# Performance work log

Measured on AMD Instinct MI355X. Metric: run time of the kernel, lower is better.

The kernel has to match this reference:

```python
import jax, jax.numpy as jnp
import numpy as np

N = 50000
E = 600000
OB_DIM = 128
H = 128
P_OUT = 8


def _glorot(key, fan_in, fan_out):
    lim = float(np.sqrt(6.0 / (fan_in + fan_out)))
    return jax.random.uniform(key, (fan_in, fan_out), jnp.float32, -lim, lim)


def setup_inputs() -> dict:
    key = jax.random.key(0)
    ks = jax.random.split(key, 16)
    x = jax.random.normal(ks[0], (N, OB_DIM), jnp.float32)
    edge_index = jax.random.randint(ks[1], (2, E), 0, N, jnp.int64)
    dims = [(OB_DIM, H), (H, H), (H, P_OUT), (OB_DIM, H), (H, H), (H, 1)]
    names = ["p1", "p2", "p3", "v1", "v2", "v3"]
    inp = {"x": x, "edge_index": edge_index}
    for i, (nm, (fi, fo)) in enumerate(zip(names, dims)):
        inp["W" + nm] = _glorot(ks[2 + i], fi, fo)
        inp["b" + nm] = jnp.zeros((fo,), jnp.float32)
    return inp


def _gcn_norm(edge_index, n):
    # add self-loops, symmetric normalization deg^{-1/2} A_hat deg^{-1/2}
    loops = jnp.arange(n, dtype=edge_index.dtype)
    src = jnp.concatenate([edge_index[0], loops])
    dst = jnp.concatenate([edge_index[1], loops])
    deg = jax.ops.segment_sum(jnp.ones_like(dst, jnp.float32), dst, num_segments=n)
    dinv = jax.lax.rsqrt(jnp.maximum(deg, 1.0))
    norm = dinv[src] * dinv[dst]  # [E+N]
    return src, dst, norm


def _gcn_conv(x, W, b, src, dst, norm, n):
    h = x @ W                      # [N, out]
    msg = h[src] * norm[:, None]   # gather + scale, [E+N, out]
    out = jax.ops.segment_sum(msg, dst, num_segments=n)
    return out + b


def reference(x, edge_index, Wp1, bp1, Wp2, bp2, Wp3, bp3, Wv1, bv1, Wv2, bv2, Wv3, bv3):
    n = x.shape[0]
    src, dst, norm = _gcn_norm(edge_index, n)
    # policy branch
    a = jax.nn.relu(_gcn_conv(x, Wp1, bp1, src, dst, norm, n))
    a = jax.nn.relu(_gcn_conv(a, Wp2, bp2, src, dst, norm, n))
    action_logits = _gcn_conv(a, Wp3, bp3, src, dst, norm, n)  # Categorical logits
    # value branch
    v = jax.nn.relu(_gcn_conv(x, Wv1, bv1, src, dst, norm, n))
    v = jax.nn.relu(_gcn_conv(v, Wv2, bv2, src, dst, norm, n))
    v = _gcn_conv(v, Wv3, bv3, src, dst, norm, n)
    return action_logits, v
```

## Files before the change

kernel.cpp:

```cpp
#include <hip/hip_runtime.h>

#define NN 50000
#define NE 600000

typedef unsigned short ushort_t;
typedef ushort_t ushortx8 __attribute__((ext_vector_type(8)));
typedef ushort_t ushortx4 __attribute__((ext_vector_type(4)));
typedef short bf16x8 __attribute__((ext_vector_type(8)));
typedef float f32x4 __attribute__((ext_vector_type(4)));
typedef int intx2 __attribute__((ext_vector_type(2)));
typedef float fltx4 __attribute__((ext_vector_type(4)));

__device__ __forceinline__ float bf2f(ushort_t u) {
    union { unsigned int i; float f; } c;
    c.i = ((unsigned int)u) << 16;
    return c.f;
}
__device__ __forceinline__ ushort_t f2bf(float f) {
    union { float f; unsigned int i; } c;
    c.f = f;
    unsigned int u = c.i;
    unsigned int r = u + 0x7FFFu + ((u >> 16) & 1u);
    return (ushort_t)(r >> 16);
}
__device__ __forceinline__ unsigned cvtpk(float lo, float hi) {
    unsigned r;
    asm("v_cvt_pk_bf16_f32 %0, %1, %2" : "=v"(r) : "v"(lo), "v"(hi));
    return r;
}

__global__ void k_pre(const float* __restrict__ X, ushort_t* __restrict__ XB,
                      const int* __restrict__ ei, int* __restrict__ cnt) {
    int b = blockIdx.x;
    if (b < 3125) {
        size_t i = (size_t)b * 256 + threadIdx.x;
        const float4* X4 = (const float4*)X;
        float4 a = X4[i * 2], c4 = X4[i * 2 + 1];
        union { unsigned u[4]; ushortx8 v; } cv;
        cv.u[0] = cvtpk(a.x, a.y);
        cv.u[1] = cvtpk(a.z, a.w);
        cv.u[2] = cvtpk(c4.x, c4.y);
        cv.u[3] = cvtpk(c4.z, c4.w);
        __builtin_nontemporal_store(cv.v, (ushortx8*)XB + i);
    } else {
        int e = (b - 3125) * 256 + threadIdx.x;
        if (e < NE) {
            int d = __builtin_nontemporal_load(ei + NE + e);
            atomicAdd(&cnt[d], 1);
        }
    }
}

__global__ void k_scan1(const int* __restrict__ cnt, int* __restrict__ rowptr,
                        int* __restrict__ bsum, float* __restrict__ dinv) {
    __shared__ int s[256];
    int t = threadIdx.x;
    int i = blockIdx.x * 256 + t;
    int v = (i < NN) ? cnt[i] : 0;
    if (i < NN) dinv[i] = rsqrtf(1.0f + (float)v);
    s[t] = v;
    __syncthreads();
    for (int d = 1; d < 256; d <<= 1) {
        int tmp = (t >= d) ? s[t - d] : 0;
        __syncthreads();
        s[t] += tmp;
        __syncthreads();
    }
    if (i < NN) rowptr[i] = s[t] - v;
    if (t == 255) bsum[blockIdx.x] = s[255];
}

__global__ void k_scan2_prep(int* __restrict__ bsum, int* __restrict__ boff, int nb,
                             const float* __restrict__ Wp1, const float* __restrict__ Wv1,
                             const float* __restrict__ Wp2, const float* __restrict__ Wv2,
                             ushort_t* __restrict__ Wt1, ushort_t* __restrict__ Wt2p,
                             ushort_t* __restrict__ Wt2v) {
    int b = blockIdx.x, t = threadIdx.x;
    if (b < 128) {
        int idx = b * 256 + t;
        int n = idx >> 7, k = idx & 127;
        float v = (n < 128) ? Wp1[k * 128 + n] : Wv1[k * 128 + (n - 128)];
        Wt1[n * 128 + k] = f2bf(v);
    } else if (b < 192) {
        int idx = (b - 128) * 256 + t;
        int n = idx >> 7, k = idx & 127;
        Wt2p[n * 128 + k] = f2bf(Wp2[k * 128 + n]);
    } else if (b < 256) {
        int idx = (b - 192) * 256 + t;
        int n = idx >> 7, k = idx & 127;
        Wt2v[n * 128 + k] = f2bf(Wv2[k * 128 + n]);
    } else {
        __shared__ int s[256];
        int v = (t < nb) ? bsum[t] : 0;
        s[t] = v;
        __syncthreads();
        for (int d = 1; d < 256; d <<= 1) {
            int tmp = (t >= d) ? s[t - d] : 0;
            __syncthreads();
            s[t] += tmp;
            __syncthreads();
        }
        boff[t] = s[t] - v;
    }
}

__global__ void k_scan3rc(const int* __restrict__ rowptr, const int* __restrict__ cnt,
                          const int* __restrict__ boff, int2* __restrict__ rc) {
    int i = blockIdx.x * 256 + threadIdx.x;
    if (i < NN) {
        int2 v;
        v.x = rowptr[i] + boff[blockIdx.x];
        v.y = cnt[i];
        rc[i] = v;
    }
}

__global__ void k_fill(const int* __restrict__ ei, const int2* __restrict__ rc,
                       int* __restrict__ fill, const float* __restrict__ dinv,
                       int2* __restrict__ edges) {
    int e = blockIdx.x * 256 + threadIdx.x;
    if (e < NE) {
        int s = __builtin_nontemporal_load(ei + e);
        int d = __builtin_nontemporal_load(ei + NE + e);
        int pos = rc[d].x + atomicAdd(&fill[d], 1);
        int2 pr;
        pr.x = s;
        pr.y = __float_as_int(dinv[s] * dinv[d]);
        edges[pos] = pr;
    }
}

__global__ __launch_bounds__(256) void k_agg128(const ushort_t* __restrict__ H,
                                                ushort_t* __restrict__ OUT,
                                                const float* __restrict__ dinv,
                                                const int2* __restrict__ rc,
                                                const int2* __restrict__ edges) {
    int wv = threadIdx.x >> 6;
    int l = threadIdx.x & 63;
    int i = blockIdx.x * 4 + wv;
    if (i >= NN) return;
    int t2 = l >> 4, q = l & 15;
    const ushortx8* H8 = (const ushortx8*)H;

    float a0[8] = {}, a1[8] = {};
    float di = dinv[i];
    float ws = (t2 == 0) ? di * di : 0.f;
    ushortx8 hv = H8[(size_t)i * 16 + q];
#pragma unroll
    for (int k = 0; k < 8; ++k) a0[k] = ws * bf2f(hv[k]);

    int2 rcv = rc[i];
    int st = rcv.x, n = rcv.y;

    for (int j = t2; j < n; j += 16) {
        int idx[4];
        float w[4];
#pragma unroll
        for (int s = 0; s < 4; ++s) {
            int jj = j + 4 * s;
            bool valid = jj < n;
            intx2 em = __builtin_nontemporal_load(
                (const intx2*)edges + (valid ? st + jj : st));
            idx[s] = valid ? em.x : i;
            w[s] = valid ? __int_as_float(em.y) : 0.f;
        }
        ushortx8 hh[4];
#pragma unroll
        for (int s = 0; s < 4; ++s) hh[s] = H8[(size_t)idx[s] * 16 + q];
#pragma unroll
        for (int k = 0; k < 8; ++k) a0[k] += w[0] * bf2f(hh[0][k]);
#pragma unroll
        for (int k = 0; k < 8; ++k) a1[k] += w[1] * bf2f(hh[1][k]);
#pragma unroll
        for (int k = 0; k < 8; ++k) a0[k] += w[2] * bf2f(hh[2][k]);
#pragma unroll
        for (int k = 0; k < 8; ++k) a1[k] += w[3] * bf2f(hh[3][k]);
    }
#pragma unroll
    for (int k = 0; k < 8; ++k) a0[k] += a1[k];
#pragma unroll
    for (int k = 0; k < 8; ++k) {
        a0[k] += __shfl_xor(a0[k], 16, 64);
        a0[k] += __shfl_xor(a0[k], 32, 64);
    }
    if (l < 16) {
        ushortx8 o = {f2bf(a0[0]), f2bf(a0[1]), f2bf(a0[2]), f2bf(a0[3]),
                      f2bf(a0[4]), f2bf(a0[5]), f2bf(a0[6]), f2bf(a0[7])};
        __builtin_nontemporal_store(o, (ushortx8*)OUT + (size_t)i * 16 + q);
    }
}

__global__ __launch_bounds__(256) void k_agg256(const ushort_t* __restrict__ H,
                                                ushort_t* __restrict__ OUT,
                                                const float* __restrict__ dinv,
                                                const int2* __restrict__ rc,
                                                const int2* __restrict__ edges) {
    int wv = threadIdx.x >> 6;
    int l = threadIdx.x & 63;
    int i = blockIdx.x * 4 + wv;
    if (i >= NN) return;
    int h = l >> 5, q = l & 31;
    const ushortx8* H8 = (const ushortx8*)H;

    float a0[8] = {}, a1[8] = {};
    float di = dinv[i];
    float ws = (h == 0) ? di * di : 0.f;
    ushortx8 hv = H8[(size_t)i * 32 + q];
#pragma unroll
    for (int k = 0; k < 8; ++k) a0[k] = ws * bf2f(hv[k]);

    int2 rcv = rc[i];
    int st = rcv.x, n = rcv.y;

    for (int j = h; j < n; j += 8) {
        int idx[4];
        float w[4];
#pragma unroll
        for (int s = 0; s < 4; ++s) {
            int jj = j + 2 * s;
            bool valid = jj < n;
            intx2 em = __builtin_nontemporal_load(
                (const intx2*)edges + (valid ? st + jj : st));
            idx[s] = valid ? em.x : i;
            w[s] = valid ? __int_as_float(em.y) : 0.f;
        }
        ushortx8 hh[4];
#pragma unroll
        for (int s = 0; s < 4; ++s) hh[s] = H8[(size_t)idx[s] * 32 + q];
#pragma unroll
        for (int k = 0; k < 8; ++k) a0[k] += w[0] * bf2f(hh[0][k]);
#pragma unroll
        for (int k = 0; k < 8; ++k) a1[k] += w[1] * bf2f(hh[1][k]);
#pragma unroll
        for (int k = 0; k < 8; ++k) a0[k] += w[2] * bf2f(hh[2][k]);
#pragma unroll
        for (int k = 0; k < 8; ++k) a1[k] += w[3] * bf2f(hh[3][k]);
    }
#pragma unroll
    for (int k = 0; k < 8; ++k) a0[k] += a1[k];
#pragma unroll
    for (int k = 0; k < 8; ++k) a0[k] += __shfl_xor(a0[k], 32, 64);

    if (h == 0) {
        ushortx8 o = {f2bf(a0[0]), f2bf(a0[1]), f2bf(a0[2]), f2bf(a0[3]),
                      f2bf(a0[4]), f2bf(a0[5]), f2bf(a0[6]), f2bf(a0[7])};
        __builtin_nontemporal_store(o, (ushortx8*)OUT + (size_t)i * 32 + q);
    }
}

__global__ __launch_bounds__(256) void k_gemm1(const ushort_t* __restrict__ A,
                                               const ushort_t* __restrict__ Wt1,
                                               const float* __restrict__ bL,
                                               const float* __restrict__ bH,
                                               ushort_t* __restrict__ C, int nrows) {
    __shared__ ushort_t Wl[256 * 128];
    int t = threadIdx.x;
    const ushortx8* Wg = (const ushortx8*)Wt1;
#pragma unroll
    for (int i = 0; i < 16; ++i) {
        int c = i * 256 + t;
        int row = c >> 4, slot = c & 15;
        int db = row * 256 + ((slot * 16) ^ ((row & 7) << 4));
        *(ushortx8*)((char*)Wl + db) = Wg[c];
    }
    __syncthreads();

    int w = t >> 6, l = t & 63, m = l & 15, g = l >> 4;
    int r0 = blockIdx.x * 64 + w * 16;
    if (r0 >= nrows) return;

    const ushort_t* Arow = A + (size_t)(r0 + m) * 128;
    bf16x8 af[4];
#pragma unroll
    for (int kk = 0; kk < 4; ++kk) af[kk] = *(const bf16x8*)(Arow + kk * 32 + g * 8);

    f32x4 acc[16];
#pragma unroll
    for (int nt = 0; nt < 16; ++nt) acc[nt] = (f32x4){0.f, 0.f, 0.f, 0.f};
    int sw = (m & 7) << 4;
#pragma unroll
    for (int nt = 0; nt < 16; ++nt) {
        const char* Wb = (const char*)Wl + (nt * 16 + m) * 256;
#pragma unroll
        for (int kk = 0; kk < 4; ++kk) {
            bf16x8 wf = *(const bf16x8*)(Wb + ((kk * 64 + g * 16) ^ sw));
            acc[nt] = __builtin_amdgcn_mfma_f32_16x16x32_bf16(wf, af[kk], acc[nt], 0, 0, 0);
        }
    }
#pragma unroll
    for (int nt = 0; nt < 16; ++nt) {
        const float* bb = (nt < 8) ? (bL + nt * 16 + g * 4) : (bH + (nt - 8) * 16 + g * 4);
        float4 bv = *(const float4*)bb;
        ushortx4 o = {f2bf(fmaxf(acc[nt][0] + bv.x, 0.f)),
                      f2bf(fmaxf(acc[nt][1] + bv.y, 0.f)),
                      f2bf(fmaxf(acc[nt][2] + bv.z, 0.f)),
                      f2bf(fmaxf(acc[nt][3] + bv.w, 0.f))};
        *(ushortx4*)(C + (size_t)(r0 + m) * 256 + nt * 16 + g * 4) = o;
    }
}

__global__ __launch_bounds__(256) void k_gemm2s(const ushort_t* __restrict__ A,
                                                const ushort_t* __restrict__ Wp,
                                                const ushort_t* __restrict__ Wv,
                                                const float* __restrict__ bL,
                                                const float* __restrict__ bH,
                                                const float* __restrict__ Wp3,
                                                const float* __restrict__ Wv3,
                                                float* __restrict__ FS, int nrows) {
    __shared__ ushort_t Wl[2 * 128 * 128];
    __shared__ float W3c[9][128];
    int t = threadIdx.x;
    const ushortx8* Wgp = (const ushortx8*)Wp;
    const ushortx8* Wgv = (const ushortx8*)Wv;
#pragma unroll
    for (int i = 0; i < 8; ++i) {
        int c = i * 256 + t;
        int row = c >> 4, slot = c & 15;
        int db = row * 256 + ((slot * 16) ^ ((row & 7) << 4));
        *(ushortx8*)((char*)Wl + db) = Wgp[c];
        *(ushortx8*)((char*)Wl + 32768 + db) = Wgv[c];
    }
    for (int jj = t; jj < 1152; jj += 256) {
        int c = jj >> 7, k = jj & 127;
        W3c[c][k] = (c < 8) ? Wp3[k * 8 + c] : Wv3[k];
    }
    __syncthreads();

    int w = t >> 6, l = t & 63, m = l & 15, g = l >> 4;
    int r0 = blockIdx.x * 64 + w * 16;
    if (r0 >= nrows) return;

    const ushort_t* Arow = A + (size_t)(r0 + m) * 256;
    bf16x8 alo[4], ahi[4];
#pragma unroll
    for (int kk = 0; kk < 4; ++kk) {
        alo[kk] = *(const bf16x8*)(Arow + kk * 32 + g * 8);
        ahi[kk] = *(const bf16x8*)(Arow + 128 + kk * 32 + g * 8);
    }

    f32x4 accp[8], accv[8];
#pragma unroll
    for (int nt = 0; nt < 8; ++nt) {
        accp[nt] = (f32x4){0.f, 0.f, 0.f, 0.f};
        accv[nt] = (f32x4){0.f, 0.f, 0.f, 0.f};
    }
    int sw = (m & 7) << 4;
#pragma unroll
    for (int nt = 0; nt < 8; ++nt) {
        const char* Wbp = (const char*)Wl + (nt * 16 + m) * 256;
        const char* Wbv = Wbp + 32768;
#pragma unroll
        for (int kk = 0; kk < 4; ++kk) {
            int off = (kk * 64 + g * 16) ^ sw;
            bf16x8 wfp = *(const bf16x8*)(Wbp + off);
            accp[nt] = __builtin_amdgcn_mfma_f32_16x16x32_bf16(wfp, alo[kk], accp[nt], 0, 0, 0);
            bf16x8 wfv = *(const bf16x8*)(Wbv + off);
            accv[nt] = __builtin_amdgcn_mfma_f32_16x16x32_bf16(wfv, ahi[kk], accv[nt], 0, 0, 0);
        }
    }

    float rp[8][4], rv[8][4];
#pragma unroll
    for (int nt = 0; nt < 8; ++nt) {
        float4 bp = *(const float4*)(bL + nt * 16 + g * 4);
        float4 bv = *(const float4*)(bH + nt * 16 + g * 4);
        rp[nt][0] = fmaxf(accp[nt][0] + bp.x, 0.f);
        rp[nt][1] = fmaxf(accp[nt][1] + bp.y, 0.f);
        rp[nt][2] = fmaxf(accp[nt][2] + bp.z, 0.f);
        rp[nt][3] = fmaxf(accp[nt][3] + bp.w, 0.f);
        rv[nt][0] = fmaxf(accv[nt][0] + bv.x, 0.f);
        rv[nt][1] = fmaxf(accv[nt][1] + bv.y, 0.f);
        rv[nt][2] = fmaxf(accv[nt][2] + bv.z, 0.f);
        rv[nt][3] = fmaxf(accv[nt][3] + bv.w, 0.f);
    }

    float ps[9] = {};
#pragma unroll
    for (int c = 0; c < 8; ++c) {
#pragma unroll
        for (int nt = 0; nt < 8; ++nt) {
            float4 w4 = *(const float4*)&W3c[c][nt * 16 + g * 4];
            ps[c] += rp[nt][0] * w4.x + rp[nt][1] * w4.y + rp[nt][2] * w4.z + rp[nt][3] * w4.w;
        }
    }
#pragma unroll
    for (int nt = 0; nt < 8; ++nt) {
        float4 w4 = *(const float4*)&W3c[8][nt * 16 + g * 4];
        ps[8] += rv[nt][0] * w4.x + rv[nt][1] * w4.y + rv[nt][2] * w4.z + rv[nt][3] * w4.w;
    }
#pragma unroll
    for (int c = 0; c < 9; ++c) {
        ps[c] += __shfl_xor(ps[c], 16, 64);
        ps[c] += __shfl_xor(ps[c], 32, 64);
    }
    if (g == 0) {
        float* o = FS + (size_t)(r0 + m) * 12;
        fltx4 o0 = {ps[0], ps[1], ps[2], ps[3]};
        fltx4 o1 = {ps[4], ps[5], ps[6], ps[7]};
        __builtin_nontemporal_store(o0, (fltx4*)o);
        __builtin_nontemporal_store(o1, (fltx4*)o + 1);
        __builtin_nontemporal_store(ps[8], o + 8);
    }
}

__global__ void k_agg9(const float* __restrict__ FS, float* __restrict__ out_logits,
                       float* __restrict__ out_v, const float* __restrict__ bp3,
                       const float* __restrict__ bv3, const float* __restrict__ dinv,
                       const int2* __restrict__ rc, const int2* __restrict__ edges) {
    int i = blockIdx.x * 256 + threadIdx.x;
    if (i >= NN) return;
    float di = dinv[i];
    float w0 = di * di;
    const float4* F = (const float4*)FS;
    size_t b0 = (size_t)i * 3;
    float4 x0 = F[b0], x1 = F[b0 + 1], x2 = F[b0 + 2];
    float a[9];
    a[0] = w0 * x0.x; a[1] = w0 * x0.y; a[2] = w0 * x0.z; a[3] = w0 * x0.w;
    a[4] = w0 * x1.x; a[5] = w0 * x1.y; a[6] = w0 * x1.z; a[7] = w0 * x1.w;
    a[8] = w0 * x2.x;
    int2 rcv = rc[i];
    int st = rcv.x, n = rcv.y;
    for (int j = 0; j < n; ++j) {
        int2 e = edges[st + j];
        float w = __int_as_float(e.y);
        size_t sb = (size_t)e.x * 3;
        float4 y0 = F[sb], y1 = F[sb + 1], y2 = F[sb + 2];
        a[0] += w * y0.x; a[1] += w * y0.y; a[2] += w * y0.z; a[3] += w * y0.w;
        a[4] += w * y1.x; a[5] += w * y1.y; a[6] += w * y1.z; a[7] += w * y1.w;
        a[8] += w * y2.x;
    }
    float4 bpa = *(const float4*)bp3;
    float4 bpb = *(const float4*)(bp3 + 4);
    fltx4 o0 = {a[0] + bpa.x, a[1] + bpa.y, a[2] + bpa.z, a[3] + bpa.w};
    fltx4 o1 = {a[4] + bpb.x, a[5] + bpb.y, a[6] + bpb.z, a[7] + bpb.w};
    __builtin_nontemporal_store(o0, (fltx4*)out_logits + (size_t)i * 2);
    __builtin_nontemporal_store(o1, (fltx4*)out_logits + (size_t)i * 2 + 1);
    __builtin_nontemporal_store(a[8] + bv3[0], out_v + i);
}

extern "C" void kernel_launch(void* const* d_in, const int* in_sizes, int n_in,
                              void* d_out, int out_size, void* d_ws, size_t ws_size,
                              hipStream_t stream) {
    const float* x   = (const float*)d_in[0];
    const int*   ei  = (const int*)d_in[1];
    const float* Wp1 = (const float*)d_in[2],  *bp1 = (const float*)d_in[3];
    const float* Wp2 = (const float*)d_in[4],  *bp2 = (const float*)d_in[5];
    const float* Wp3 = (const float*)d_in[6],  *bp3 = (const float*)d_in[7];
    const float* Wv1 = (const float*)d_in[8],  *bv1 = (const float*)d_in[9];
    const float* Wv2 = (const float*)d_in[10], *bv2 = (const float*)d_in[11];
    const float* Wv3 = (const float*)d_in[12], *bv3 = (const float*)d_in[13];
    float* out_logits = (float*)d_out;
    float* out_v = (float*)d_out + (size_t)NN * 8;

    char* w = (char*)d_ws;
    auto alloc = [&](size_t bytes) {
        char* p = w;
        w += (bytes + 255) & ~(size_t)255;
        return p;
    };
    int*      cntfill = (int*)alloc((size_t)2 * NN * 4);
    int*      cnt    = cntfill;
    int*      fill   = cntfill + NN;
    int*      rowptr = (int*)alloc(NN * 4);
    int*      bsum   = (int*)alloc(256 * 4);
    int*      boff   = (int*)alloc(256 * 4);
    float*    dinv   = (float*)alloc(NN * 4);
    int2*     rc     = (int2*)alloc((size_t)NN * 8);
    int2*     edges  = (int2*)alloc((size_t)NE * 8);
    ushort_t* Wt1    = (ushort_t*)alloc(256 * 128 * 2);
    ushort_t* Wt2p   = (ushort_t*)alloc(128 * 128 * 2);
    ushort_t* Wt2v   = (ushort_t*)alloc(128 * 128 * 2);
    ushort_t* xb     = (ushort_t*)alloc((size_t)NN * 128 * 2);
    ushort_t* ag0    = (ushort_t*)alloc((size_t)NN * 128 * 2);
    ushort_t* f1b    = (ushort_t*)alloc((size_t)NN * 256 * 2);
    ushort_t* ag1    = (ushort_t*)alloc((size_t)NN * 256 * 2);
    float*    fs     = (float*)alloc((size_t)NN * 12 * 4);

    const int NB = (NN + 255) / 256;
    const int EB = (NE + 255) / 256;
    const int GB = (NN + 63) / 64;
    const int AB = NN / 4;

    (void)hipMemsetAsync(cntfill, 0, (size_t)2 * NN * 4, stream);
    k_pre<<<3125 + EB, 256, 0, stream>>>(x, xb, ei, cnt);
    k_scan1<<<NB, 256, 0, stream>>>(cnt, rowptr, bsum, dinv);
    k_scan2_prep<<<257, 256, 0, stream>>>(bsum, boff, NB, Wp1, Wv1, Wp2, Wv2,
                                          Wt1, Wt2p, Wt2v);
    k_scan3rc<<<NB, 256, 0, stream>>>(rowptr, cnt, boff, rc);
    k_fill<<<EB, 256, 0, stream>>>(ei, rc, fill, dinv, edges);

    k_agg128<<<AB, 256, 0, stream>>>(xb, ag0, dinv, rc, edges);
    k_gemm1<<<GB, 256, 0, stream>>>(ag0, Wt1, bp1, bv1, f1b, NN);
    k_agg256<<<AB, 256, 0, stream>>>(f1b, ag1, dinv, rc, edges);
    k_gemm2s<<<GB, 256, 0, stream>>>(ag1, Wt2p, Wt2v, bp2, bv2, Wp3, Wv3, fs, NN);
    k_agg9<<<NB, 256, 0, stream>>>(fs, out_logits, out_v, bp3, bv3, dinv, rc, edges);
}
```

Before: 207.0 us.

## Merge CSR scan kernels with atomic block offsets and fold weight prep into preprocess

The three-kernel prefix scan becomes a single kernel. Each block takes its global row offset from an atomic counter, which leaves CSR segments out of node order but still valid. The weight transpose and bf16 conversion move into the preprocessing kernel, cutting two launches and their serialization. Nontemporal stores on intermediates become regular stores so later kernels can hit them in cache, and the final feature buffer is padded from 12 to 16 floats per row for aligned gathers. The costs are non-deterministic edge ordering across nodes and extra memory for the padded buffer.

```diff
diff --git a/kernel.cpp b/kernel.cpp
--- a/kernel.cpp
+++ b/kernel.cpp
@@ -2,6 +2,7 @@
 
 #define NN 50000
 #define NE 600000
+#define EBLK 2344
 
 typedef unsigned short ushort_t;
 typedef ushort_t ushortx8 __attribute__((ext_vector_type(8)));
@@ -30,10 +31,14 @@
 }
 
 __global__ void k_pre(const float* __restrict__ X, ushort_t* __restrict__ XB,
-                      const int* __restrict__ ei, int* __restrict__ cnt) {
-    int b = blockIdx.x;
+                      const int* __restrict__ ei, int* __restrict__ cnt,
+                      const float* __restrict__ Wp1, const float* __restrict__ Wv1,
+                      const float* __restrict__ Wp2, const float* __restrict__ Wv2,
+                      ushort_t* __restrict__ Wt1, ushort_t* __restrict__ Wt2p,
+                      ushort_t* __restrict__ Wt2v) {
+    int b = blockIdx.x, t = threadIdx.x;
     if (b < 3125) {
-        size_t i = (size_t)b * 256 + threadIdx.x;
+        size_t i = (size_t)b * 256 + t;
         const float4* X4 = (const float4*)X;
         float4 a = X4[i * 2], c4 = X4[i * 2 + 1];
         union { unsigned u[4]; ushortx8 v; } cv;
@@ -41,19 +46,36 @@
         cv.u[1] = cvtpk(a.z, a.w);
         cv.u[2] = cvtpk(c4.x, c4.y);
         cv.u[3] = cvtpk(c4.z, c4.w);
-        __builtin_nontemporal_store(cv.v, (ushortx8*)XB + i);
-    } else {
-        int e = (b - 3125) * 256 + threadIdx.x;
+        ((ushortx8*)XB)[i] = cv.v;
+    } else if (b < 3125 + EBLK) {
+        int e = (b - 3125) * 256 + t;
         if (e < NE) {
             int d = __builtin_nontemporal_load(ei + NE + e);
             atomicAdd(&cnt[d], 1);
         }
-    }
-}
-
-__global__ void k_scan1(const int* __restrict__ cnt, int* __restrict__ rowptr,
-                        int* __restrict__ bsum, float* __restrict__ dinv) {
+    } else {
+        int wb = b - 3125 - EBLK;
+        if (wb < 128) {
+            int idx = wb * 256 + t;
+            int n = idx >> 7, k = idx & 127;
+            float v = (n < 128) ? Wp1[k * 128 + n] : Wv1[k * 128 + (n - 128)];
+            Wt1[n * 128 + k] = f2bf(v);
+        } else if (wb < 192) {
+            int idx = (wb - 128) * 256 + t;
+            int n = idx >> 7, k = idx & 127;
+            Wt2p[n * 128 + k] = f2bf(Wp2[k * 128 + n]);
+        } else {
+            int idx = (wb - 192) * 256 + t;
+            int n = idx >> 7, k = idx & 127;
+            Wt2v[n * 128 + k] = f2bf(Wv2[k * 128 + n]);
+        }
+    }
+}
+
+__global__ void k_scanrc(const int* __restrict__ cnt, float* __restrict__ dinv,
+                         int2* __restrict__ rc, int* __restrict__ gofs) {
     __shared__ int s[256];
+    __shared__ int base;
     int t = threadIdx.x;
     int i = blockIdx.x * 256 + t;
     int v = (i < NN) ? cnt[i] : 0;
@@ -66,52 +88,13 @@
         s[t] += tmp;
         __syncthreads();
     }
-    if (i < NN) rowptr[i] = s[t] - v;
-    if (t == 255) bsum[blockIdx.x] = s[255];
-}
-
-__global__ void k_scan2_prep(int* __restrict__ bsum, int* __restrict__ boff, int nb,
-                             const float* __restrict__ Wp1, const float* __restrict__ Wv1,
-                             const float* __restrict__ Wp2, const float* __restrict__ Wv2,
-                             ushort_t* __restrict__ Wt1, ushort_t* __restrict__ Wt2p,
-                             ushort_t* __restrict__ Wt2v) {
-    int b = blockIdx.x, t = threadIdx.x;
-    if (b < 128) {
-        int idx = b * 256 + t;
-        int n = idx >> 7, k = idx & 127;
-        float v = (n < 128) ? Wp1[k * 128 + n] : Wv1[k * 128 + (n - 128)];
-        Wt1[n * 128 + k] = f2bf(v);
-    } else if (b < 192) {
-        int idx = (b - 128) * 256 + t;
-        int n = idx >> 7, k = idx & 127;
-        Wt2p[n * 128 + k] = f2bf(Wp2[k * 128 + n]);
-    } else if (b < 256) {
-        int idx = (b - 192) * 256 + t;
-        int n = idx >> 7, k = idx & 127;
-        Wt2v[n * 128 + k] = f2bf(Wv2[k * 128 + n]);
-    } else {
-        __shared__ int s[256];
-        int v = (t < nb) ? bsum[t] : 0;
-        s[t] = v;
-        __syncthreads();
-        for (int d = 1; d < 256; d <<= 1) {
-            int tmp = (t >= d) ? s[t - d] : 0;
-            __syncthreads();
-            s[t] += tmp;
-            __syncthreads();
-        }
-        boff[t] = s[t] - v;
-    }
-}
-
-__global__ void k_scan3rc(const int* __restrict__ rowptr, const int* __restrict__ cnt,
-                          const int* __restrict__ boff, int2* __restrict__ rc) {
-    int i = blockIdx.x * 256 + threadIdx.x;
+    if (t == 255) base = atomicAdd(gofs, s[255]);
+    __syncthreads();
     if (i < NN) {
-        int2 v;
-        v.x = rowptr[i] + boff[blockIdx.x];
-        v.y = cnt[i];
-        rc[i] = v;
+        int2 o;
+        o.x = base + s[t] - v;
+        o.y = v;
+        rc[i] = o;
     }
 }
 
@@ -186,7 +169,7 @@
     if (l < 16) {
         ushortx8 o = {f2bf(a0[0]), f2bf(a0[1]), f2bf(a0[2]), f2bf(a0[3]),
                       f2bf(a0[4]), f2bf(a0[5]), f2bf(a0[6]), f2bf(a0[7])};
-        __builtin_nontemporal_store(o, (ushortx8*)OUT + (size_t)i * 16 + q);
+        ((ushortx8*)OUT)[(size_t)i * 16 + q] = o;
     }
 }
 
@@ -244,7 +227,7 @@
     if (h == 0) {
         ushortx8 o = {f2bf(a0[0]), f2bf(a0[1]), f2bf(a0[2]), f2bf(a0[3]),
                       f2bf(a0[4]), f2bf(a0[5]), f2bf(a0[6]), f2bf(a0[7])};
-        __builtin_nontemporal_store(o, (ushortx8*)OUT + (size_t)i * 32 + q);
+        ((ushortx8*)OUT)[(size_t)i * 32 + q] = o;
     }
 }
 
@@ -394,12 +377,10 @@
         ps[c] += __shfl_xor(ps[c], 32, 64);
     }
     if (g == 0) {
-        float* o = FS + (size_t)(r0 + m) * 12;
-        fltx4 o0 = {ps[0], ps[1], ps[2], ps[3]};
-        fltx4 o1 = {ps[4], ps[5], ps[6], ps[7]};
-        __builtin_nontemporal_store(o0, (fltx4*)o);
-        __builtin_nontemporal_store(o1, (fltx4*)o + 1);
-        __builtin_nontemporal_store(ps[8], o + 8);
+        float* o = FS + (size_t)(r0 + m) * 16;
+        *(fltx4*)o = (fltx4){ps[0], ps[1], ps[2], ps[3]};
+        *(fltx4*)(o + 4) = (fltx4){ps[4], ps[5], ps[6], ps[7]};
+        o[8] = ps[8];
     }
 }
 
@@ -412,22 +393,24 @@
     float di = dinv[i];
     float w0 = di * di;
     const float4* F = (const float4*)FS;
-    size_t b0 = (size_t)i * 3;
-    float4 x0 = F[b0], x1 = F[b0 + 1], x2 = F[b0 + 2];
+    size_t b0 = (size_t)i * 4;
+    float4 x0 = F[b0], x1 = F[b0 + 1];
+    float x2 = FS[(size_t)i * 16 + 8];
     float a[9];
     a[0] = w0 * x0.x; a[1] = w0 * x0.y; a[2] = w0 * x0.z; a[3] = w0 * x0.w;
     a[4] = w0 * x1.x; a[5] = w0 * x1.y; a[6] = w0 * x1.z; a[7] = w0 * x1.w;
-    a[8] = w0 * x2.x;
+    a[8] = w0 * x2;
     int2 rcv = rc[i];
     int st = rcv.x, n = rcv.y;
     for (int j = 0; j < n; ++j) {
         int2 e = edges[st + j];
         float w = __int_as_float(e.y);
-        size_t sb = (size_t)e.x * 3;
-        float4 y0 = F[sb], y1 = F[sb + 1], y2 = F[sb + 2];
+        size_t sb = (size_t)e.x * 4;
+        float4 y0 = F[sb], y1 = F[sb + 1];
+        float y2 = FS[(size_t)e.x * 16 + 8];
         a[0] += w * y0.x; a[1] += w * y0.y; a[2] += w * y0.z; a[3] += w * y0.w;
         a[4] += w * y1.x; a[5] += w * y1.y; a[6] += w * y1.z; a[7] += w * y1.w;
-        a[8] += w * y2.x;
+        a[8] += w * y2;
     }
     float4 bpa = *(const float4*)bp3;
     float4 bpb = *(const float4*)(bp3 + 4);
@@ -458,12 +441,10 @@
         w += (bytes + 255) & ~(size_t)255;
         return p;
     };
-    int*      cntfill = (int*)alloc((size_t)2 * NN * 4);
-    int*      cnt    = cntfill;
-    int*      fill   = cntfill + NN;
-    int*      rowptr = (int*)alloc(NN * 4);
-    int*      bsum   = (int*)alloc(256 * 4);
-    int*      boff   = (int*)alloc(256 * 4);
+    int*      zeroed = (int*)alloc(((size_t)2 * NN + 256) * 4);
+    int*      cnt    = zeroed;
+    int*      fill   = zeroed + NN;
+    int*      gofs   = zeroed + 2 * NN;
     float*    dinv   = (float*)alloc(NN * 4);
     int2*     rc     = (int2*)alloc((size_t)NN * 8);
     int2*     edges  = (int2*)alloc((size_t)NE * 8);
@@ -474,20 +455,17 @@
     ushort_t* ag0    = (ushort_t*)alloc((size_t)NN * 128 * 2);
     ushort_t* f1b    = (ushort_t*)alloc((size_t)NN * 256 * 2);
     ushort_t* ag1    = (ushort_t*)alloc((size_t)NN * 256 * 2);
-    float*    fs     = (float*)alloc((size_t)NN * 12 * 4);
+    float*    fs     = (float*)alloc((size_t)NN * 16 * 4);
 
     const int NB = (NN + 255) / 256;
-    const int EB = (NE + 255) / 256;
     const int GB = (NN + 63) / 64;
     const int AB = NN / 4;
 
-    (void)hipMemsetAsync(cntfill, 0, (size_t)2 * NN * 4, stream);
-    k_pre<<<3125 + EB, 256, 0, stream>>>(x, xb, ei, cnt);
-    k_scan1<<<NB, 256, 0, stream>>>(cnt, rowptr, bsum, dinv);
-    k_scan2_prep<<<257, 256, 0, stream>>>(bsum, boff, NB, Wp1, Wv1, Wp2, Wv2,
-                                          Wt1, Wt2p, Wt2v);
-    k_scan3rc<<<NB, 256, 0, stream>>>(rowptr, cnt, boff, rc);
-    k_fill<<<EB, 256, 0, stream>>>(ei, rc, fill, dinv, edges);
+    (void)hipMemsetAsync(zeroed, 0, ((size_t)2 * NN + 256) * 4, stream);
+    k_pre<<<3125 + EBLK + 256, 256, 0, stream>>>(x, xb, ei, cnt, Wp1, Wv1, Wp2, Wv2,
+                                                 Wt1, Wt2p, Wt2v);
+    k_scanrc<<<NB, 256, 0, stream>>>(cnt, dinv, rc, gofs);
+    k_fill<<<EBLK, 256, 0, stream>>>(ei, rc, fill, dinv, edges);
 
     k_agg128<<<AB, 256, 0, stream>>>(xb, ag0, dinv, rc, edges);
     k_gemm1<<<GB, 256, 0, stream>>>(ag0, Wt1, bp1, bv1, f1b, NN);
```

Measured after the change: 202.9 us, median of 2. 2.0% less time.
